# Performance work log

Hardware: AMD Instinct MI355X
Metric: run time of the kernel (lower is better)

Reference implementation:

```python
import jax, jax.numpy as jnp
import numpy as np

N = 100000   # nodes
E = 1600000  # edges
D = 128      # in_channels
H = 128      # hidden_dim
L = 3        # num_layers
LH = 128     # lstm_hidden
OUT = 16     # output_dim
G = 128      # graphs in batch
EPS = 1e-5   # BatchNorm eps


def setup_inputs() -> dict:
    key = jax.random.key(0)
    ks = jax.random.split(key, 14)
    x = jax.random.normal(ks[0], (N, D), jnp.float32)
    src = jax.random.randint(ks[1], (E,), 0, N)
    dst = jax.random.randint(ks[2], (E,), 0, N)
    edge_index = jnp.stack([src, dst])
    batch = jnp.sort(jax.random.randint(ks[3], (N,), 0, G))
    Ws = jax.random.normal(ks[4], (L, D, H), jnp.float32) / np.float32(np.sqrt(D))
    bs = jax.random.normal(ks[5], (L, H), jnp.float32) * 0.02
    gammas = 1.0 + 0.1 * jax.random.normal(ks[6], (L, H), jnp.float32)
    betas = 0.1 * jax.random.normal(ks[7], (L, H), jnp.float32)
    rms = 0.1 * jax.random.normal(ks[8], (L, H), jnp.float32)
    rvs = jax.random.uniform(ks[9], (L, H), jnp.float32, 0.5, 1.5)
    W_ih = jax.random.normal(ks[10], (4 * LH, H), jnp.float32) / np.float32(np.sqrt(H))
    W_hh = jax.random.normal(ks[11], (4 * LH, LH), jnp.float32) / np.float32(np.sqrt(LH))
    b_ih = jnp.zeros((4 * LH,), jnp.float32)
    b_hh = jnp.zeros((4 * LH,), jnp.float32)
    W_fc = jax.random.normal(ks[12], (OUT, LH), jnp.float32) / np.float32(np.sqrt(LH))
    b_fc = 0.02 * jax.random.normal(ks[13], (OUT,), jnp.float32)
    return dict(x=x, edge_index=edge_index, batch=batch, Ws=Ws, bs=bs,
                gammas=gammas, betas=betas, rms=rms, rvs=rvs,
                W_ih=W_ih, W_hh=W_hh, b_ih=b_ih, b_hh=b_hh, W_fc=W_fc, b_fc=b_fc)


def reference(x, edge_index, batch, Ws, bs, gammas, betas, rms, rvs,
              W_ih, W_hh, b_ih, b_hh, W_fc, b_fc):
    # GCNConv: add self-loops, symmetric deg^-1/2 normalization
    src, dst = edge_index[0], edge_index[1]
    loop = jnp.arange(N)
    s = jnp.concatenate([src, loop])
    d = jnp.concatenate([dst, loop])
    deg = jax.ops.segment_sum(jnp.ones((E + N,), x.dtype), d, num_segments=N)
    dinv = jax.lax.rsqrt(jnp.maximum(deg, 1.0))  # deg >= 1 due to self-loops
    norm = (dinv[s] * dinv[d])[:, None]          # [E+N, 1]
    h = x
    for l in range(L):
        h = h @ Ws[l]                                                  # [N, H]
        agg = jax.ops.segment_sum(h[s] * norm, d, num_segments=N) + bs[l]
        # BatchNorm (eval: running stats) -> dropout (eval: identity) -> ReLU
        y = (agg - rms[l]) * (gammas[l] * jax.lax.rsqrt(rvs[l] + EPS)) + betas[l]
        h = jax.nn.relu(y)
    # global_mean_pool
    sums = jax.ops.segment_sum(h, batch, num_segments=G)               # [G, H]
    cnt = jax.ops.segment_sum(jnp.ones((N,), h.dtype), batch, num_segments=G)
    pooled = sums / jnp.maximum(cnt, 1.0)[:, None]
    # single-timestep LSTM, h0 = c0 = 0 -> forget gate contributes nothing
    gates = pooled @ W_ih.T + b_ih + b_hh                              # [G, 4*LH]
    i, f, g, o = jnp.split(gates, 4, axis=-1)
    c = jax.nn.sigmoid(i) * jnp.tanh(g)
    hn = jax.nn.sigmoid(o) * jnp.tanh(c)
    return hn @ W_fc.T + b_fc                                          # [G, OUT]
```

## Files before the change

### kernel.cpp

```cpp
#include <hip/hip_runtime.h>
#include <math.h>

constexpr int   NN  = 100000;
constexpr int   EE  = 1600000;
constexpr int   HH  = 128;
constexpr int   GG  = 128;
constexpr float EPSV = 1e-5f;
constexpr int   NSB = 256;
constexpr int   SUBW = (NN + NSB - 1) / NSB;
constexpr int   CAP2 = 8192;
constexpr int   GEMM_BLOCKS = (NN + 127) / 128;
constexpr int   WHALF = 64 * 136;
constexpr int   WLAYER = 2 * 2 * WHALF;

typedef __attribute__((ext_vector_type(8))) short  short8;
typedef __attribute__((ext_vector_type(4))) float  f32x4;
typedef __attribute__((ext_vector_type(2))) float  v2f;

__device__ __forceinline__ unsigned short f2bf(float f) {
    union { float f; unsigned u; } v; v.f = f;
    unsigned r = v.u + 0x7FFF + ((v.u >> 16) & 1);
    return (unsigned short)(r >> 16);
}
__device__ __forceinline__ float bf2f(unsigned short b) {
    union { unsigned u; float f; } v; v.u = ((unsigned)b) << 16;
    return v.f;
}

constexpr size_t A256(size_t x) { return (x + 255) & ~(size_t)255; }
constexpr size_t OFF_TL  = 0;
constexpr size_t OFF_DNV = A256(OFF_TL  + 256 * 4);
constexpr size_t OFF_RP  = A256(OFF_DNV + (size_t)NN * 4);
constexpr size_t OFF_SRC = A256(OFF_RP  + (size_t)(NN + 1) * 4);
constexpr size_t OFF_B2  = A256(OFF_SRC + (size_t)EE * 4);
constexpr size_t OFF_ED  = A256(OFF_B2  + (size_t)NSB * CAP2 * 4);
constexpr size_t OFF_WS  = A256(OFF_ED  + (size_t)EE * 8);
constexpr size_t OFF_HW  = A256(OFF_WS  + (size_t)2 * WLAYER * 2);
constexpr size_t OFF_H0  = A256(OFF_HW  + (size_t)NN * HH * 2);
constexpr size_t OFF_PL  = A256(OFF_H0  + (size_t)NN * HH * 2);

template<bool FP32A>
__device__ __forceinline__ void gemm_body(const void* __restrict__ Ap,
                                          const float* __restrict__ W,
                                          const unsigned short* __restrict__ Wsp,
                                          unsigned short* __restrict__ C,
                                          int nrows, int rb) {
    __shared__ unsigned short smem[2 * WHALF];
    unsigned short* WtH = smem;
    unsigned short* WtL = smem + WHALF;
    int t = threadIdx.x;
    int row0 = rb * 128;
    int wv = t >> 6, lane = t & 63, m = lane & 15, q = lane >> 4;
    long rowA = row0 + wv * 32 + m;
    long rowB = rowA + 16;

    short8 a[2][4];
#pragma unroll
    for (int kc = 0; kc < 4; ++kc) {
        int ko = kc * 32 + q * 8;
        if (FP32A) {
            const float* Af = (const float*)Ap;
            float4 f0 = {0,0,0,0}, f1 = {0,0,0,0}, g0 = {0,0,0,0}, g1 = {0,0,0,0};
            if (rowA < nrows) {
                f0 = *(const float4*)(Af + rowA * 128 + ko);
                f1 = *(const float4*)(Af + rowA * 128 + ko + 4);
            }
            if (rowB < nrows) {
                g0 = *(const float4*)(Af + rowB * 128 + ko);
                g1 = *(const float4*)(Af + rowB * 128 + ko + 4);
            }
            union { short8 s; unsigned short u[8]; } ua, ub;
            ua.u[0] = f2bf(f0.x); ua.u[1] = f2bf(f0.y); ua.u[2] = f2bf(f0.z); ua.u[3] = f2bf(f0.w);
            ua.u[4] = f2bf(f1.x); ua.u[5] = f2bf(f1.y); ua.u[6] = f2bf(f1.z); ua.u[7] = f2bf(f1.w);
            ub.u[0] = f2bf(g0.x); ub.u[1] = f2bf(g0.y); ub.u[2] = f2bf(g0.z); ub.u[3] = f2bf(g0.w);
            ub.u[4] = f2bf(g1.x); ub.u[5] = f2bf(g1.y); ub.u[6] = f2bf(g1.z); ub.u[7] = f2bf(g1.w);
            a[0][kc] = ua.s; a[1][kc] = ub.s;
        } else {
            const unsigned short* Ab = (const unsigned short*)Ap;
            short8 z = {};
            a[0][kc] = (rowA < nrows) ? *(const short8*)(Ab + rowA * 128 + ko) : z;
            a[1][kc] = (rowB < nrows) ? *(const short8*)(Ab + rowB * 128 + ko) : z;
        }
    }

    for (int half = 0; half < 2; ++half) {
        int c0 = half * 64;
        __syncthreads();
        if (FP32A) {
            for (int idx = t; idx < 64 * 128; idx += 256) {
                int k = idx >> 6, c = idx & 63;
                float w = W[k * 128 + c0 + c];
                unsigned short hb = f2bf(w);
                WtH[c * 136 + k] = hb;
                WtL[c * 136 + k] = f2bf(w - bf2f(hb));
            }
        } else {
            const uint4* srcw = (const uint4*)(Wsp + (size_t)half * 2 * WHALF);
            uint4* dstw = (uint4*)smem;
            for (int i = t; i < 2176; i += 256) dstw[i] = srcw[i];
        }
        __syncthreads();
        f32x4 acc[2][4] = {};
#pragma unroll
        for (int kc = 0; kc < 4; ++kc) {
            int ko = kc * 32 + q * 8;
#pragma unroll
            for (int ct = 0; ct < 4; ++ct) {
                short8 bh = *(const short8*)(WtH + (ct * 16 + m) * 136 + ko);
                short8 bl = *(const short8*)(WtL + (ct * 16 + m) * 136 + ko);
                acc[0][ct] = __builtin_amdgcn_mfma_f32_16x16x32_bf16(a[0][kc], bh, acc[0][ct], 0, 0, 0);
                acc[0][ct] = __builtin_amdgcn_mfma_f32_16x16x32_bf16(a[0][kc], bl, acc[0][ct], 0, 0, 0);
                acc[1][ct] = __builtin_amdgcn_mfma_f32_16x16x32_bf16(a[1][kc], bh, acc[1][ct], 0, 0, 0);
                acc[1][ct] = __builtin_amdgcn_mfma_f32_16x16x32_bf16(a[1][kc], bl, acc[1][ct], 0, 0, 0);
            }
        }
        __syncthreads();
        unsigned short* Cs = smem;
#pragma unroll
        for (int rt = 0; rt < 2; ++rt)
#pragma unroll
            for (int ct = 0; ct < 4; ++ct)
#pragma unroll
                for (int r = 0; r < 4; ++r) {
                    int rl = wv * 32 + rt * 16 + q * 4 + r;
                    Cs[rl * 68 + ct * 16 + m] = f2bf(acc[rt][ct][r]);
                }
        __syncthreads();
        for (int idx = t; idx < 128 * 16; idx += 256) {
            int row = idx >> 4, ch = idx & 15;
            long grow = row0 + row;
            if (grow < nrows)
                *(ushort4*)(C + grow * 128 + c0 + ch * 4) = *(const ushort4*)(Cs + row * 68 + ch * 4);
        }
    }
}

__device__ void binall_body(const int* __restrict__ src, const int* __restrict__ dst,
                            unsigned* __restrict__ bins2, unsigned* __restrict__ tail2,
                            int b) {
    __shared__ unsigned cnt[NSB];
    __shared__ unsigned cur[NSB];
    int t = threadIdx.x;
    cnt[t] = 0;
    __syncthreads();
    const int nvec = EE / 4;
    int csz = (nvec + NSB - 1) / NSB;
    int i0 = b * csz;
    int i1 = i0 + csz; if (i1 > nvec) i1 = nvec;
    const int4* d4 = (const int4*)dst;
    const int4* s4 = (const int4*)src;
    for (int i = i0 + t; i < i1; i += 256) {
        int4 d = d4[i];
        atomicAdd(&cnt[(unsigned)d.x / SUBW], 1u);
        atomicAdd(&cnt[(unsigned)d.y / SUBW], 1u);
        atomicAdd(&cnt[(unsigned)d.z / SUBW], 1u);
        atomicAdd(&cnt[(unsigned)d.w / SUBW], 1u);
    }
    __syncthreads();
    cur[t] = atomicAdd(&tail2[t], cnt[t]);
    __syncthreads();
    for (int i = i0 + t; i < i1; i += 256) {
        int4 d = d4[i];
        int4 s = s4[i];
        int dd[4] = {d.x, d.y, d.z, d.w};
        int ss[4] = {s.x, s.y, s.z, s.w};
#pragma unroll
        for (int c = 0; c < 4; ++c) {
            unsigned gsb = (unsigned)dd[c] / SUBW;
            unsigned p = atomicAdd(&cur[gsb], 1u);
            if (p < (unsigned)CAP2)
                bins2[(size_t)gsb * CAP2 + p] =
                    ((unsigned)(dd[c] - gsb * SUBW) << 17) | (unsigned)ss[c];
        }
    }
}

__global__ __launch_bounds__(256) void k_gemm0_bin(const float* __restrict__ x,
                                                   const float* __restrict__ W,
                                                   unsigned short* __restrict__ C,
                                                   const int* __restrict__ src,
                                                   const int* __restrict__ dst,
                                                   unsigned* __restrict__ bins2,
                                                   unsigned* __restrict__ tail2) {
    if (blockIdx.x < GEMM_BLOCKS)
        gemm_body<true>(x, W, nullptr, C, NN, blockIdx.x);
    else
        binall_body(src, dst, bins2, tail2, blockIdx.x - GEMM_BLOCKS);
}

__global__ __launch_bounds__(256) void k_gemm(const unsigned short* __restrict__ A,
                                              const unsigned short* __restrict__ Wsp,
                                              unsigned short* __restrict__ C) {
    gemm_body<false>(A, nullptr, Wsp, C, NN, blockIdx.x);
}

__global__ __launch_bounds__(256) void k_build(const unsigned* __restrict__ bins2,
                                               const unsigned* __restrict__ tail2,
                                               int* __restrict__ rp,
                                               float* __restrict__ dinv,
                                               int* __restrict__ ssrc,
                                               float* __restrict__ pooled,
                                               const float* __restrict__ Ws,
                                               unsigned short* __restrict__ wsp) {
    int b = blockIdx.x, t = threadIdx.x;

    if (b >= NSB) {
        int e = (b - NSB) * 256 + t;
        int l = e >> 14;
        int r = e & 16383;
        int k = r >> 7;
        int c = r & 127;
        int half = c >> 6, cl = c & 63;
        float w = Ws[(size_t)(l + 1) * 16384 + k * 128 + c];
        unsigned short hb = f2bf(w);
        unsigned short lb = f2bf(w - bf2f(hb));
        size_t base = (size_t)l * WLAYER + (size_t)half * 2 * WHALF;
        wsp[base + cl * 136 + k]         = hb;
        wsp[base + WHALF + cl * 136 + k] = lb;
        return;
    }

    __shared__ int hist[SUBW];
    __shared__ int sa[512], sd[512];
    __shared__ unsigned ta[256], tb[256];

    if (b < 65) {
        int idx = b * 256 + t;
        if (idx < GG * HH + GG) pooled[idx] = 0.f;
    }

    unsigned v = tail2[t];
    ta[t] = v;
    __syncthreads();
    unsigned *sp = ta, *dp = tb;
    for (int off = 1; off < 256; off <<= 1) {
        dp[t] = sp[t] + ((t >= off) ? sp[t - off] : 0u);
        __syncthreads();
        unsigned* tmp = sp; sp = dp; dp = tmp;
    }
    unsigned base = sp[b] - tail2[b];
    unsigned m = tail2[b];
    if (m > (unsigned)CAP2) m = CAP2;

    int lo = b * SUBW;
    int nn = NN - lo; if (nn > SUBW) nn = SUBW;
    for (int i = t; i < nn; i += 256) hist[i] = 0;
    __syncthreads();

    const unsigned* bb = bins2 + (size_t)b * CAP2;
    unsigned nv = m >> 2;
    for (unsigned i = t; i < nv; i += 256) {
        uint4 u = ((const uint4*)bb)[i];
        atomicAdd(&hist[u.x >> 17], 1);
        atomicAdd(&hist[u.y >> 17], 1);
        atomicAdd(&hist[u.z >> 17], 1);
        atomicAdd(&hist[u.w >> 17], 1);
    }
    for (unsigned i = (m & ~3u) + t; i < m; i += 256)
        atomicAdd(&hist[bb[i] >> 17], 1);
    __syncthreads();

    sa[t]       = (t < nn)       ? hist[t]       : 0;
    sa[t + 256] = (t + 256 < nn) ? hist[t + 256] : 0;
    __syncthreads();
    int* s = sa; int* d = sd;
    for (int off = 1; off < 512; off <<= 1) {
        d[t]       = s[t]       + ((t >= off)       ? s[t - off]       : 0);
        d[t + 256] = s[t + 256] + ((t + 256 >= off) ? s[t + 256 - off] : 0);
        __syncthreads();
        int* tmp = s; s = d; d = tmp;
    }

    for (int i = t; i < nn; i += 256) {
        int cur0 = (int)base + (i ? s[i - 1] : 0);
        rp[lo + i]   = cur0;
        dinv[lo + i] = rsqrtf((float)(hist[i] + 1));
    }
    __syncthreads();
    for (int i = t; i < nn; i += 256)
        hist[i] = (int)base + (i ? s[i - 1] : 0);
    if (b == 255 && t == 0) rp[NN] = EE;
    __syncthreads();

    for (unsigned i = t; i < nv; i += 256) {
        uint4 u = ((const uint4*)bb)[i];
        int p;
        p = atomicAdd(&hist[u.x >> 17], 1); ssrc[p] = (int)(u.x & 0x1FFFFu);
        p = atomicAdd(&hist[u.y >> 17], 1); ssrc[p] = (int)(u.y & 0x1FFFFu);
        p = atomicAdd(&hist[u.z >> 17], 1); ssrc[p] = (int)(u.z & 0x1FFFFu);
        p = atomicAdd(&hist[u.w >> 17], 1); ssrc[p] = (int)(u.w & 0x1FFFFu);
    }
    for (unsigned i = (m & ~3u) + t; i < m; i += 256) {
        unsigned u = bb[i];
        int p = atomicAdd(&hist[u >> 17], 1);
        ssrc[p] = (int)(u & 0x1FFFFu);
    }
}

template<bool WRITE_ED>
__global__ __launch_bounds__(256) void k_agg(const unsigned short* __restrict__ hw,
                                             const int* __restrict__ rp,
                                             const int* __restrict__ ssrc,
                                             uint2* __restrict__ edata,
                                             const float* __restrict__ dinv,
                                             const float* __restrict__ bsl,
                                             const float* __restrict__ gamma,
                                             const float* __restrict__ beta,
                                             const float* __restrict__ rm,
                                             const float* __restrict__ rv,
                                             unsigned short* __restrict__ out) {
    int lane = threadIdx.x & 63;
    int c2   = lane * 2;
    int n = blockIdx.x * 4 + (threadIdx.x >> 6);
    if (n >= NN) return;
    int beg = rp[n], end = rp[n + 1];

    v2f acc0 = {0.f, 0.f}, acc1 = {0.f, 0.f};

    for (int chunk = beg; chunk < end; chunk += 64) {
        int l = chunk + lane;
        int   e;
        float dv;
        if (WRITE_ED) {
            bool valid = (l < end);
            e  = valid ? ssrc[l] : n;
            dv = valid ? dinv[e] : 0.f;
            if (valid) edata[l] = make_uint2((unsigned)e, __float_as_uint(dv));
        } else {
            uint2 ed = (l < end) ? ((const uint2*)edata)[l] : make_uint2((unsigned)n, 0u);
            e  = (int)ed.x;
            dv = __uint_as_float(ed.y);
        }
        int cnt = end - chunk;
        if (cnt > 64) cnt = 64;
        for (int jb = 0; jb < cnt; jb += 8) {
#pragma unroll
            for (int j = 0; j < 8; ++j) {
                int s    = __builtin_amdgcn_readlane(e, jb + j);
                float ds = __int_as_float(
                               __builtin_amdgcn_readlane(__float_as_int(dv), jb + j));
                unsigned u = *(const unsigned*)(hw + (size_t)s * HH + c2);
                v2f vv;
                vv.x = __int_as_float((int)(u << 16));
                vv.y = __int_as_float((int)(u & 0xffff0000u));
                v2f d2 = {ds, ds};
                if (j & 1) acc1 += d2 * vv;
                else       acc0 += d2 * vv;
            }
        }
    }
    v2f a = acc0 + acc1;

    float di = dinv[n];
    {
        unsigned u = *(const unsigned*)(hw + (size_t)n * HH + c2);
        v2f vv;
        vv.x = __int_as_float((int)(u << 16));
        vv.y = __int_as_float((int)(u & 0xffff0000u));
        v2f d2 = {di, di};
        a += d2 * vv;
    }
    a.x *= di;
    a.y *= di;

    float g0 = gamma[c2],   g1 = gamma[c2 + 1];
    float r0 = rv[c2],      r1 = rv[c2 + 1];
    float s0 = g0 * rsqrtf(r0 + EPSV);
    float s1 = g1 * rsqrtf(r1 + EPSV);
    float b0 = fmaf(bsl[c2]     - rm[c2],     s0, beta[c2]);
    float b1 = fmaf(bsl[c2 + 1] - rm[c2 + 1], s1, beta[c2 + 1]);
    float y0 = fmaxf(fmaf(a.x, s0, b0), 0.f);
    float y1 = fmaxf(fmaf(a.y, s1, b1), 0.f);
    ushort2 o;
    o.x = f2bf(y0);
    o.y = f2bf(y1);
    *(ushort2*)(out + (size_t)n * HH + c2) = o;
}

__global__ __launch_bounds__(128) void k_pool(const unsigned short* __restrict__ h,
                                              const int* __restrict__ batch,
                                              float* __restrict__ pooled,
                                              float* __restrict__ cnt) {
    int t = threadIdx.x;
    const int chunk = (NN + 2047) / 2048;
    int n0 = blockIdx.x * chunk;
    if (n0 >= NN) return;
    int n1 = n0 + chunk;
    if (n1 > NN) n1 = NN;
    int cur = batch[n0];
    float acc = 0.f;
    int k = 0;
    for (int n = n0; n < n1; ++n) {
        int b = batch[n];
        if (b != cur) {
            atomicAdd(&pooled[(size_t)cur * 128 + t], acc);
            if (t == 0) atomicAdd(&cnt[cur], (float)k);
            acc = 0.f; k = 0; cur = b;
        }
        acc += bf2f(h[(size_t)n * 128 + t]);
        ++k;
    }
    atomicAdd(&pooled[(size_t)cur * 128 + t], acc);
    if (t == 0) atomicAdd(&cnt[cur], (float)k);
}

__global__ __launch_bounds__(128) void k_head(const float* __restrict__ pooled,
                                              const float* __restrict__ cnt,
                                              const float* __restrict__ W_ih,
                                              const float* __restrict__ b_ih,
                                              const float* __restrict__ b_hh,
                                              const float* __restrict__ W_fc,
                                              const float* __restrict__ b_fc,
                                              float* __restrict__ out) {
    __shared__ float pm[128];
    __shared__ float gate[512];
    __shared__ float hn[128];
    int g = blockIdx.x, t = threadIdx.x;
    float cdiv = fmaxf(cnt[g], 1.0f);
    pm[t] = pooled[(size_t)g * 128 + t] / cdiv;
    __syncthreads();
    for (int j = t; j < 512; j += 128) {
        float acc = b_ih[j] + b_hh[j];
        const float* w = W_ih + (size_t)j * 128;
#pragma unroll 8
        for (int k = 0; k < 128; ++k) acc = fmaf(pm[k], w[k], acc);
        gate[j] = acc;
    }
    __syncthreads();
    {
        float gi = gate[t], gg = gate[256 + t], go = gate[384 + t];
        float cc = (1.f / (1.f + expf(-gi))) * tanhf(gg);
        hn[t] = (1.f / (1.f + expf(-go))) * tanhf(cc);
    }
    __syncthreads();
    if (t < 16) {
        float acc = b_fc[t];
        const float* w = W_fc + (size_t)t * 128;
#pragma unroll 8
        for (int k = 0; k < 128; ++k) acc = fmaf(hn[k], w[k], acc);
        out[(size_t)g * 16 + t] = acc;
    }
}

extern "C" void kernel_launch(void* const* d_in, const int* in_sizes, int n_in,
                              void* d_out, int out_size, void* d_ws, size_t ws_size,
                              hipStream_t stream) {
    const float* x      = (const float*)d_in[0];
    const int*   ei     = (const int*)d_in[1];
    const int*   src    = ei;
    const int*   dst    = ei + EE;
    const int*   batch  = (const int*)d_in[2];
    const float* Ws     = (const float*)d_in[3];
    const float* bs     = (const float*)d_in[4];
    const float* gammas = (const float*)d_in[5];
    const float* betas  = (const float*)d_in[6];
    const float* rms    = (const float*)d_in[7];
    const float* rvs    = (const float*)d_in[8];
    const float* W_ih   = (const float*)d_in[9];
    const float* b_ih   = (const float*)d_in[11];
    const float* b_hh   = (const float*)d_in[12];
    const float* W_fc   = (const float*)d_in[13];
    const float* b_fc   = (const float*)d_in[14];
    float* out = (float*)d_out;

    char* w = (char*)d_ws;
    unsigned*       tail2  = (unsigned*)(w + OFF_TL);
    float*          dinv   = (float*)(w + OFF_DNV);
    int*            rp     = (int*)(w + OFF_RP);
    int*            ssrc   = (int*)(w + OFF_SRC);
    unsigned*       bins2  = (unsigned*)(w + OFF_B2);
    uint2*          edata  = (uint2*)(w + OFF_ED);
    unsigned short* wsp    = (unsigned short*)(w + OFF_WS);
    unsigned short* hwb    = (unsigned short*)(w + OFF_HW);
    unsigned short* h0     = (unsigned short*)(w + OFF_H0);
    float*          pooled = (float*)(w + OFF_PL);
    float*          cntb   = pooled + (size_t)GG * HH;

    hipMemsetAsync(tail2, 0, 256 * 4, stream);

    k_gemm0_bin<<<GEMM_BLOCKS + NSB, 256, 0, stream>>>(x, Ws, hwb, src, dst, bins2, tail2);
    k_build<<<NSB + 128, 256, 0, stream>>>(bins2, tail2, rp, dinv, ssrc, pooled, Ws, wsp);

    for (int l = 0; l < 3; ++l) {
        if (l > 0)
            k_gemm<<<GEMM_BLOCKS, 256, 0, stream>>>(h0, wsp + (size_t)(l - 1) * WLAYER, hwb);
        if (l == 0)
            k_agg<true><<<(NN + 3) / 4, 256, 0, stream>>>(hwb, rp, ssrc, edata, dinv,
                                                          bs, gammas, betas, rms, rvs, h0);
        else
            k_agg<false><<<(NN + 3) / 4, 256, 0, stream>>>(hwb, rp, ssrc, edata, dinv,
                                                           bs + l * 128, gammas + l * 128,
                                                           betas + l * 128, rms + l * 128,
                                                           rvs + l * 128, h0);
    }
    k_pool<<<2048, 128, 0, stream>>>(h0, batch, pooled, cntb);
    k_head<<<GG, 128, 0, stream>>>(pooled, cntb, W_ih, b_ih, b_hh, W_fc, b_fc, out);
}
```

Before: 420.4 us.

## Gather 16-byte row slices across four concurrent edges per wave in aggregation

The aggregation kernel is restructured so each wave splits into four 16-lane groups. Each group processes a different edge at the same time, and each lane loads 8 bf16 channels with one 16-byte load instead of 4 bytes per lane per edge. Partial sums from the four groups are combined with cross-lane shuffles, and the BatchNorm epilogue is vectorised. This is meant to cut the per-edge serial readlane loop and raise the number of outstanding memory requests in the gather. In exchange it adds a shuffle reduction, does redundant epilogue work in three of the four groups, and issues per-lane edge-index loads instead of coalesced chunk loads.

```diff
diff --git a/kernel.cpp b/kernel.cpp
--- a/kernel.cpp
+++ b/kernel.cpp
@@ -310,71 +310,96 @@
                                              const float* __restrict__ rv,
                                              unsigned short* __restrict__ out) {
     int lane = threadIdx.x & 63;
-    int c2   = lane * 2;
+    int p    = lane & 15;
+    int gq   = lane >> 4;
     int n = blockIdx.x * 4 + (threadIdx.x >> 6);
     if (n >= NN) return;
     int beg = rp[n], end = rp[n + 1];
-
-    v2f acc0 = {0.f, 0.f}, acc1 = {0.f, 0.f};
-
-    for (int chunk = beg; chunk < end; chunk += 64) {
-        int l = chunk + lane;
-        int   e;
-        float dv;
-        if (WRITE_ED) {
-            bool valid = (l < end);
-            e  = valid ? ssrc[l] : n;
-            dv = valid ? dinv[e] : 0.f;
-            if (valid) edata[l] = make_uint2((unsigned)e, __float_as_uint(dv));
-        } else {
-            uint2 ed = (l < end) ? ((const uint2*)edata)[l] : make_uint2((unsigned)n, 0u);
-            e  = (int)ed.x;
-            dv = __uint_as_float(ed.y);
-        }
-        int cnt = end - chunk;
-        if (cnt > 64) cnt = 64;
-        for (int jb = 0; jb < cnt; jb += 8) {
-#pragma unroll
-            for (int j = 0; j < 8; ++j) {
-                int s    = __builtin_amdgcn_readlane(e, jb + j);
-                float ds = __int_as_float(
-                               __builtin_amdgcn_readlane(__float_as_int(dv), jb + j));
-                unsigned u = *(const unsigned*)(hw + (size_t)s * HH + c2);
-                v2f vv;
-                vv.x = __int_as_float((int)(u << 16));
-                vv.y = __int_as_float((int)(u & 0xffff0000u));
-                v2f d2 = {ds, ds};
-                if (j & 1) acc1 += d2 * vv;
-                else       acc0 += d2 * vv;
+    int c0 = p * 8;
+
+    v2f a0 = {0.f, 0.f}, a1 = {0.f, 0.f}, a2 = {0.f, 0.f}, a3 = {0.f, 0.f};
+
+    for (int chunk = beg; chunk < end; chunk += 16) {
+#pragma unroll
+        for (int jj = 0; jj < 4; ++jj) {
+            int e = chunk + jj * 4 + gq;
+            bool valid = (e < end);
+            int ec = valid ? e : (end - 1);
+            int s; float dv;
+            if (WRITE_ED) {
+                s  = ssrc[ec];
+                float dl = dinv[s];
+                dv = valid ? dl : 0.f;
+                if (valid && p == 0)
+                    edata[e] = make_uint2((unsigned)s, __float_as_uint(dl));
+            } else {
+                uint2 ed = edata[ec];
+                s  = (int)ed.x;
+                dv = valid ? __uint_as_float(ed.y) : 0.f;
             }
-        }
-    }
-    v2f a = acc0 + acc1;
+            uint4 u = *(const uint4*)(hw + (size_t)s * HH + c0);
+            v2f d2 = {dv, dv};
+            v2f vv;
+            vv.x = __int_as_float((int)(u.x << 16));
+            vv.y = __int_as_float((int)(u.x & 0xffff0000u));
+            a0 += d2 * vv;
+            vv.x = __int_as_float((int)(u.y << 16));
+            vv.y = __int_as_float((int)(u.y & 0xffff0000u));
+            a1 += d2 * vv;
+            vv.x = __int_as_float((int)(u.z << 16));
+            vv.y = __int_as_float((int)(u.z & 0xffff0000u));
+            a2 += d2 * vv;
+            vv.x = __int_as_float((int)(u.w << 16));
+            vv.y = __int_as_float((int)(u.w & 0xffff0000u));
+            a3 += d2 * vv;
+        }
+    }
+
+#pragma unroll
+    for (int off = 16; off < 64; off <<= 1) {
+        a0.x += __shfl_xor(a0.x, off); a0.y += __shfl_xor(a0.y, off);
+        a1.x += __shfl_xor(a1.x, off); a1.y += __shfl_xor(a1.y, off);
+        a2.x += __shfl_xor(a2.x, off); a2.y += __shfl_xor(a2.y, off);
+        a3.x += __shfl_xor(a3.x, off); a3.y += __shfl_xor(a3.y, off);
+    }
 
     float di = dinv[n];
-    {
-        unsigned u = *(const unsigned*)(hw + (size_t)n * HH + c2);
-        v2f vv;
-        vv.x = __int_as_float((int)(u << 16));
-        vv.y = __int_as_float((int)(u & 0xffff0000u));
-        v2f d2 = {di, di};
-        a += d2 * vv;
-    }
-    a.x *= di;
-    a.y *= di;
-
-    float g0 = gamma[c2],   g1 = gamma[c2 + 1];
-    float r0 = rv[c2],      r1 = rv[c2 + 1];
-    float s0 = g0 * rsqrtf(r0 + EPSV);
-    float s1 = g1 * rsqrtf(r1 + EPSV);
-    float b0 = fmaf(bsl[c2]     - rm[c2],     s0, beta[c2]);
-    float b1 = fmaf(bsl[c2 + 1] - rm[c2 + 1], s1, beta[c2 + 1]);
-    float y0 = fmaxf(fmaf(a.x, s0, b0), 0.f);
-    float y1 = fmaxf(fmaf(a.y, s1, b1), 0.f);
-    ushort2 o;
-    o.x = f2bf(y0);
-    o.y = f2bf(y1);
-    *(ushort2*)(out + (size_t)n * HH + c2) = o;
+    uint4 uh = *(const uint4*)(hw + (size_t)n * HH + c0);
+    float r8[8];
+    r8[0] = a0.x + di * bf2f((unsigned short)(uh.x & 0xffffu));
+    r8[1] = a0.y + di * bf2f((unsigned short)(uh.x >> 16));
+    r8[2] = a1.x + di * bf2f((unsigned short)(uh.y & 0xffffu));
+    r8[3] = a1.y + di * bf2f((unsigned short)(uh.y >> 16));
+    r8[4] = a2.x + di * bf2f((unsigned short)(uh.z & 0xffffu));
+    r8[5] = a2.y + di * bf2f((unsigned short)(uh.z >> 16));
+    r8[6] = a3.x + di * bf2f((unsigned short)(uh.w & 0xffffu));
+    r8[7] = a3.y + di * bf2f((unsigned short)(uh.w >> 16));
+    float4 gm0 = *(const float4*)(gamma + c0), gm1 = *(const float4*)(gamma + c0 + 4);
+    float4 rv0 = *(const float4*)(rv + c0),    rv1 = *(const float4*)(rv + c0 + 4);
+    float4 bb0 = *(const float4*)(bsl + c0),   bb1 = *(const float4*)(bsl + c0 + 4);
+    float4 rm0 = *(const float4*)(rm + c0),    rm1 = *(const float4*)(rm + c0 + 4);
+    float4 bt0 = *(const float4*)(beta + c0),  bt1 = *(const float4*)(beta + c0 + 4);
+    float gms[8] = {gm0.x, gm0.y, gm0.z, gm0.w, gm1.x, gm1.y, gm1.z, gm1.w};
+    float rvs8[8] = {rv0.x, rv0.y, rv0.z, rv0.w, rv1.x, rv1.y, rv1.z, rv1.w};
+    float bbs[8] = {bb0.x, bb0.y, bb0.z, bb0.w, bb1.x, bb1.y, bb1.z, bb1.w};
+    float rms8[8] = {rm0.x, rm0.y, rm0.z, rm0.w, rm1.x, rm1.y, rm1.z, rm1.w};
+    float bts[8] = {bt0.x, bt0.y, bt0.z, bt0.w, bt1.x, bt1.y, bt1.z, bt1.w};
+    unsigned short ob[8];
+#pragma unroll
+    for (int j = 0; j < 8; ++j) {
+        float sc = gms[j] * rsqrtf(rvs8[j] + EPSV);
+        float bj = fmaf(bbs[j] - rms8[j], sc, bts[j]);
+        float y  = fmaxf(fmaf(r8[j] * di, sc, bj), 0.f);
+        ob[j] = f2bf(y);
+    }
+    if (gq == 0) {
+        uint4 o;
+        o.x = (unsigned)ob[0] | ((unsigned)ob[1] << 16);
+        o.y = (unsigned)ob[2] | ((unsigned)ob[3] << 16);
+        o.z = (unsigned)ob[4] | ((unsigned)ob[5] << 16);
+        o.w = (unsigned)ob[6] | ((unsigned)ob[7] << 16);
+        *(uint4*)(out + (size_t)n * HH + c0) = o;
+    }
 }
 
 __global__ __launch_bounds__(128) void k_pool(const unsigned short* __restrict__ h,
```

Result: slower. 501.7 us (+19.3%).

## Split wavefront into two half-waves gathering different edges with 8-byte loads

Applied to the files above, without the earlier changes.

The aggregation kernel now has each 32-lane half of a wavefront process alternate edges, with every lane loading 4 bf16 channels (8 bytes) instead of 2. Partial sums are combined across halves with a cross-lane xor shuffle at the end, and edge data now stores a precomputed byte offset (src<<8) rather than the node index. The goal is to double the number of independent gather rows in flight per instruction and widen each memory access, so latency hiding on the random neighbour gathers improves. In exchange it uses ds_bpermute shuffles instead of readlane broadcasts, adds a final reduction, and leaves half the lanes idle during the store.

```diff
diff --git a/kernel.cpp b/kernel.cpp
--- a/kernel.cpp
+++ b/kernel.cpp
@@ -310,71 +310,97 @@
                                              const float* __restrict__ rv,
                                              unsigned short* __restrict__ out) {
     int lane = threadIdx.x & 63;
-    int c2   = lane * 2;
+    int half = lane >> 5;
+    int c4   = (lane & 31) * 4;
+    unsigned coff = (unsigned)c4 * 2;
     int n = blockIdx.x * 4 + (threadIdx.x >> 6);
     if (n >= NN) return;
     int beg = rp[n], end = rp[n + 1];
 
-    v2f acc0 = {0.f, 0.f}, acc1 = {0.f, 0.f};
+    f32x4 accA = {0.f, 0.f, 0.f, 0.f}, accB = {0.f, 0.f, 0.f, 0.f};
+    const char* hwb = (const char*)hw;
 
     for (int chunk = beg; chunk < end; chunk += 64) {
         int l = chunk + lane;
-        int   e;
+        unsigned ro;
         float dv;
         if (WRITE_ED) {
             bool valid = (l < end);
-            e  = valid ? ssrc[l] : n;
-            dv = valid ? dinv[e] : 0.f;
-            if (valid) edata[l] = make_uint2((unsigned)e, __float_as_uint(dv));
+            int e = valid ? ssrc[l] : n;
+            float dl = dinv[e];
+            dv = valid ? dl : 0.f;
+            ro = (unsigned)e << 8;
+            if (valid) edata[l] = make_uint2(ro, __float_as_uint(dl));
         } else {
-            uint2 ed = (l < end) ? ((const uint2*)edata)[l] : make_uint2((unsigned)n, 0u);
-            e  = (int)ed.x;
+            uint2 ed = (l < end) ? ((const uint2*)edata)[l]
+                                 : make_uint2((unsigned)n << 8, 0u);
+            ro = ed.x;
             dv = __uint_as_float(ed.y);
         }
         int cnt = end - chunk;
         if (cnt > 64) cnt = 64;
-        for (int jb = 0; jb < cnt; jb += 8) {
-#pragma unroll
-            for (int j = 0; j < 8; ++j) {
-                int s    = __builtin_amdgcn_readlane(e, jb + j);
-                float ds = __int_as_float(
-                               __builtin_amdgcn_readlane(__float_as_int(dv), jb + j));
-                unsigned u = *(const unsigned*)(hw + (size_t)s * HH + c2);
-                v2f vv;
-                vv.x = __int_as_float((int)(u << 16));
-                vv.y = __int_as_float((int)(u & 0xffff0000u));
-                v2f d2 = {ds, ds};
-                if (j & 1) acc1 += d2 * vv;
-                else       acc0 += d2 * vv;
+        for (int jb = 0; jb < cnt; jb += 16) {
+#pragma unroll
+            for (int p = 0; p < 8; ++p) {
+                int idx = jb + 2 * p + half;
+                unsigned roP = (unsigned)__shfl((int)ro, idx);
+                float    dvP = __shfl(dv, idx);
+                uint2 u = *(const uint2*)(hwb + (size_t)roP + coff);
+                float v0 = __int_as_float((int)(u.x << 16));
+                float v1 = __int_as_float((int)(u.x & 0xffff0000u));
+                float v2 = __int_as_float((int)(u.y << 16));
+                float v3 = __int_as_float((int)(u.y & 0xffff0000u));
+                if (p & 1) {
+                    accB[0] = fmaf(dvP, v0, accB[0]);
+                    accB[1] = fmaf(dvP, v1, accB[1]);
+                    accB[2] = fmaf(dvP, v2, accB[2]);
+                    accB[3] = fmaf(dvP, v3, accB[3]);
+                } else {
+                    accA[0] = fmaf(dvP, v0, accA[0]);
+                    accA[1] = fmaf(dvP, v1, accA[1]);
+                    accA[2] = fmaf(dvP, v2, accA[2]);
+                    accA[3] = fmaf(dvP, v3, accA[3]);
+                }
             }
         }
     }
-    v2f a = acc0 + acc1;
+
+    float a0 = accA[0] + accB[0];
+    float a1 = accA[1] + accB[1];
+    float a2 = accA[2] + accB[2];
+    float a3 = accA[3] + accB[3];
+    a0 += __shfl_xor(a0, 32);
+    a1 += __shfl_xor(a1, 32);
+    a2 += __shfl_xor(a2, 32);
+    a3 += __shfl_xor(a3, 32);
 
     float di = dinv[n];
-    {
-        unsigned u = *(const unsigned*)(hw + (size_t)n * HH + c2);
-        v2f vv;
-        vv.x = __int_as_float((int)(u << 16));
-        vv.y = __int_as_float((int)(u & 0xffff0000u));
-        v2f d2 = {di, di};
-        a += d2 * vv;
-    }
-    a.x *= di;
-    a.y *= di;
-
-    float g0 = gamma[c2],   g1 = gamma[c2 + 1];
-    float r0 = rv[c2],      r1 = rv[c2 + 1];
-    float s0 = g0 * rsqrtf(r0 + EPSV);
-    float s1 = g1 * rsqrtf(r1 + EPSV);
-    float b0 = fmaf(bsl[c2]     - rm[c2],     s0, beta[c2]);
-    float b1 = fmaf(bsl[c2 + 1] - rm[c2 + 1], s1, beta[c2 + 1]);
-    float y0 = fmaxf(fmaf(a.x, s0, b0), 0.f);
-    float y1 = fmaxf(fmaf(a.y, s1, b1), 0.f);
-    ushort2 o;
-    o.x = f2bf(y0);
-    o.y = f2bf(y1);
-    *(ushort2*)(out + (size_t)n * HH + c2) = o;
+    uint2 uh = *(const uint2*)(hw + (size_t)n * HH + c4);
+    a0 = (a0 + di * bf2f((unsigned short)(uh.x & 0xffffu))) * di;
+    a1 = (a1 + di * bf2f((unsigned short)(uh.x >> 16)))     * di;
+    a2 = (a2 + di * bf2f((unsigned short)(uh.y & 0xffffu))) * di;
+    a3 = (a3 + di * bf2f((unsigned short)(uh.y >> 16)))     * di;
+
+    float4 gm  = *(const float4*)(gamma + c4);
+    float4 rvv = *(const float4*)(rv + c4);
+    float4 bbv = *(const float4*)(bsl + c4);
+    float4 rmv = *(const float4*)(rm + c4);
+    float4 btv = *(const float4*)(beta + c4);
+    float s0 = gm.x * rsqrtf(rvv.x + EPSV);
+    float s1 = gm.y * rsqrtf(rvv.y + EPSV);
+    float s2 = gm.z * rsqrtf(rvv.z + EPSV);
+    float s3 = gm.w * rsqrtf(rvv.w + EPSV);
+    float y0 = fmaxf(fmaf(a0, s0, fmaf(bbv.x - rmv.x, s0, btv.x)), 0.f);
+    float y1 = fmaxf(fmaf(a1, s1, fmaf(bbv.y - rmv.y, s1, btv.y)), 0.f);
+    float y2 = fmaxf(fmaf(a2, s2, fmaf(bbv.z - rmv.z, s2, btv.z)), 0.f);
+    float y3 = fmaxf(fmaf(a3, s3, fmaf(bbv.w - rmv.w, s3, btv.w)), 0.f);
+
+    if (half == 0) {
+        uint2 o;
+        o.x = (unsigned)f2bf(y0) | ((unsigned)f2bf(y1) << 16);
+        o.y = (unsigned)f2bf(y2) | ((unsigned)f2bf(y3) << 16);
+        *(uint2*)(out + (size_t)n * HH + c4) = o;
+    }
 }
 
 __global__ __launch_bounds__(128) void k_pool(const unsigned short* __restrict__ h,
```

New measurement: 433.2 us. 1.03x slower.

## Fuse mean-pool accumulation into last aggregation layer and compute counts by binary search

Applied to the files above, without the earlier changes.

The final aggregation kernel now accumulates ReLU outputs directly into per-graph pooled sums with float atomics instead of writing bf16 node features, and the separate pooling kernel is removed. Per-graph node counts are computed in an extra build block by binary searching the sorted batch vector. This removes the last feature-map write and reread plus one launch, at the cost of many contended global atomics on a small pooled buffer and nondeterministic summation order.

```diff
diff --git a/kernel.cpp b/kernel.cpp
--- a/kernel.cpp
+++ b/kernel.cpp
@@ -201,8 +201,25 @@
                                                int* __restrict__ ssrc,
                                                float* __restrict__ pooled,
                                                const float* __restrict__ Ws,
-                                               unsigned short* __restrict__ wsp) {
+                                               unsigned short* __restrict__ wsp,
+                                               const int* __restrict__ batch,
+                                               float* __restrict__ cnt) {
     int b = blockIdx.x, t = threadIdx.x;
+
+    if (b == NSB + 128) {
+        __shared__ int lb[129];
+        if (t <= 128) {
+            int lo = 0, hi = NN;
+            while (lo < hi) {
+                int mid = (lo + hi) >> 1;
+                if (batch[mid] < t) lo = mid + 1; else hi = mid;
+            }
+            lb[t] = lo;
+        }
+        __syncthreads();
+        if (t < 128) cnt[t] = (float)(lb[t + 1] - lb[t]);
+        return;
+    }
 
     if (b >= NSB) {
         int e = (b - NSB) * 256 + t;
@@ -213,10 +230,10 @@
         int half = c >> 6, cl = c & 63;
         float w = Ws[(size_t)(l + 1) * 16384 + k * 128 + c];
         unsigned short hb = f2bf(w);
-        unsigned short lb = f2bf(w - bf2f(hb));
+        unsigned short lb2 = f2bf(w - bf2f(hb));
         size_t base = (size_t)l * WLAYER + (size_t)half * 2 * WHALF;
         wsp[base + cl * 136 + k]         = hb;
-        wsp[base + WHALF + cl * 136 + k] = lb;
+        wsp[base + WHALF + cl * 136 + k] = lb2;
         return;
     }
 
@@ -224,9 +241,8 @@
     __shared__ int sa[512], sd[512];
     __shared__ unsigned ta[256], tb[256];
 
-    if (b < 65) {
-        int idx = b * 256 + t;
-        if (idx < GG * HH + GG) pooled[idx] = 0.f;
+    if (b < 64) {
+        pooled[b * 256 + t] = 0.f;
     }
 
     unsigned v = tail2[t];
@@ -297,7 +313,7 @@
     }
 }
 
-template<bool WRITE_ED>
+template<bool WRITE_ED, bool POOL>
 __global__ __launch_bounds__(256) void k_agg(const unsigned short* __restrict__ hw,
                                              const int* __restrict__ rp,
                                              const int* __restrict__ ssrc,
@@ -308,7 +324,9 @@
                                              const float* __restrict__ beta,
                                              const float* __restrict__ rm,
                                              const float* __restrict__ rv,
-                                             unsigned short* __restrict__ out) {
+                                             unsigned short* __restrict__ out,
+                                             const int* __restrict__ batch,
+                                             float* __restrict__ pooled) {
     int lane = threadIdx.x & 63;
     int c2   = lane * 2;
     int n = blockIdx.x * 4 + (threadIdx.x >> 6);
@@ -371,37 +389,16 @@
     float b1 = fmaf(bsl[c2 + 1] - rm[c2 + 1], s1, beta[c2 + 1]);
     float y0 = fmaxf(fmaf(a.x, s0, b0), 0.f);
     float y1 = fmaxf(fmaf(a.y, s1, b1), 0.f);
-    ushort2 o;
-    o.x = f2bf(y0);
-    o.y = f2bf(y1);
-    *(ushort2*)(out + (size_t)n * HH + c2) = o;
-}
-
-__global__ __launch_bounds__(128) void k_pool(const unsigned short* __restrict__ h,
-                                              const int* __restrict__ batch,
-                                              float* __restrict__ pooled,
-                                              float* __restrict__ cnt) {
-    int t = threadIdx.x;
-    const int chunk = (NN + 2047) / 2048;
-    int n0 = blockIdx.x * chunk;
-    if (n0 >= NN) return;
-    int n1 = n0 + chunk;
-    if (n1 > NN) n1 = NN;
-    int cur = batch[n0];
-    float acc = 0.f;
-    int k = 0;
-    for (int n = n0; n < n1; ++n) {
-        int b = batch[n];
-        if (b != cur) {
-            atomicAdd(&pooled[(size_t)cur * 128 + t], acc);
-            if (t == 0) atomicAdd(&cnt[cur], (float)k);
-            acc = 0.f; k = 0; cur = b;
-        }
-        acc += bf2f(h[(size_t)n * 128 + t]);
-        ++k;
-    }
-    atomicAdd(&pooled[(size_t)cur * 128 + t], acc);
-    if (t == 0) atomicAdd(&cnt[cur], (float)k);
+    if (POOL) {
+        int bg = batch[n];
+        atomicAdd(&pooled[(size_t)bg * 128 + c2],     y0);
+        atomicAdd(&pooled[(size_t)bg * 128 + c2 + 1], y1);
+    } else {
+        ushort2 o;
+        o.x = f2bf(y0);
+        o.y = f2bf(y1);
+        *(ushort2*)(out + (size_t)n * HH + c2) = o;
+    }
 }
 
 __global__ __launch_bounds__(128) void k_head(const float* __restrict__ pooled,
@@ -479,20 +476,26 @@
     hipMemsetAsync(tail2, 0, 256 * 4, stream);
 
     k_gemm0_bin<<<GEMM_BLOCKS + NSB, 256, 0, stream>>>(x, Ws, hwb, src, dst, bins2, tail2);
-    k_build<<<NSB + 128, 256, 0, stream>>>(bins2, tail2, rp, dinv, ssrc, pooled, Ws, wsp);
+    k_build<<<NSB + 129, 256, 0, stream>>>(bins2, tail2, rp, dinv, ssrc, pooled, Ws, wsp,
+                                           batch, cntb);
 
     for (int l = 0; l < 3; ++l) {
         if (l > 0)
             k_gemm<<<GEMM_BLOCKS, 256, 0, stream>>>(h0, wsp + (size_t)(l - 1) * WLAYER, hwb);
         if (l == 0)
-            k_agg<true><<<(NN + 3) / 4, 256, 0, stream>>>(hwb, rp, ssrc, edata, dinv,
-                                                          bs, gammas, betas, rms, rvs, h0);
+            k_agg<true, false><<<(NN + 3) / 4, 256, 0, stream>>>(hwb, rp, ssrc, edata, dinv,
+                                                                 bs, gammas, betas, rms, rvs, h0,
+                                                                 batch, pooled);
+        else if (l == 1)
+            k_agg<false, false><<<(NN + 3) / 4, 256, 0, stream>>>(hwb, rp, ssrc, edata, dinv,
+                                                                  bs + 128, gammas + 128,
+                                                                  betas + 128, rms + 128,
+                                                                  rvs + 128, h0, batch, pooled);
         else
-            k_agg<false><<<(NN + 3) / 4, 256, 0, stream>>>(hwb, rp, ssrc, edata, dinv,
-                                                           bs + l * 128, gammas + l * 128,
-                                                           betas + l * 128, rms + l * 128,
-                                                           rvs + l * 128, h0);
-    }
-    k_pool<<<2048, 128, 0, stream>>>(h0, batch, pooled, cntb);
+            k_agg<false, true><<<(NN + 3) / 4, 256, 0, stream>>>(hwb, rp, ssrc, edata, dinv,
+                                                                 bs + 256, gammas + 256,
+                                                                 betas + 256, rms + 256,
+                                                                 rvs + 256, h0, batch, pooled);
+    }
     k_head<<<GG, 128, 0, stream>>>(pooled, cntb, W_ih, b_ih, b_hh, W_fc, b_fc, out);
 }
```

After: 541.6 us. 28.8% more time.
